# Kernel tuning notes

Hardware: AMD Instinct MI355X
Metric: run time of the kernel (lower is better)

Reference implementation:

```python
import jax, jax.numpy as jnp
import numpy as np

B, S, D, H = 4, 1024, 1024, 16
DK = D // H
EPS = 1e-6


def setup_inputs() -> dict:
    key = jax.random.key(0)
    ks = jax.random.split(key, 12)
    s = 1.0 / np.sqrt(D)
    inp = {
        "query": jax.random.normal(ks[0], (B, S, D), jnp.float32),
        "key": jax.random.normal(ks[1], (B, S, D), jnp.float32),
        "value": jax.random.normal(ks[2], (B, S, D), jnp.float32),
        "Wq": jax.random.normal(ks[3], (D, D), jnp.float32) * s,
        "bq": jnp.zeros((D,), jnp.float32),
        "Wk": jax.random.normal(ks[4], (D, D), jnp.float32) * s,
        "bk": jnp.zeros((D,), jnp.float32),
        "Wv": jax.random.normal(ks[5], (D, D), jnp.float32) * s,
        "bv": jnp.zeros((D,), jnp.float32),
        "Wo": jax.random.normal(ks[6], (D, D), jnp.float32) * s,
        "bo": jnp.zeros((D,), jnp.float32),
        "gamma": jnp.ones((D,), jnp.float32),
        "beta": jnp.zeros((D,), jnp.float32),
    }
    return inp


def reference(query, key, value, Wq, bq, Wk, bk, Wv, bv, Wo, bo, gamma, beta):
    residual = query
    # QKV projections, split into heads: [B,S,D] -> [B,H,S,DK]
    q = (query @ Wq + bq).reshape(B, S, H, DK).transpose(0, 2, 1, 3)
    k = (key @ Wk + bk).reshape(B, S, H, DK).transpose(0, 2, 1, 3)
    v = (value @ Wv + bv).reshape(B, S, H, DK).transpose(0, 2, 1, 3)
    # scaled dot-product attention (dropout is identity in eval mode)
    scores = jnp.einsum("bhqd,bhkd->bhqk", q, k) / jnp.sqrt(jnp.float32(DK))
    attn = jax.nn.softmax(scores, axis=-1)  # [B,H,S,S]
    x = jnp.einsum("bhqk,bhkd->bhqd", attn, v)
    x = x.transpose(0, 2, 1, 3).reshape(B, S, D)
    # residual + LayerNorm(eps=1e-6)
    x = x + residual
    mu = jnp.mean(x, axis=-1, keepdims=True)
    var = jnp.mean(jnp.square(x - mu), axis=-1, keepdims=True)
    x = (x - mu) * jax.lax.rsqrt(var + EPS) * gamma + beta
    out = x @ Wo + bo
    return (out, attn)
```

## Files before the change

kernel.cpp:

```cpp
#include <hip/hip_runtime.h>

typedef unsigned short u16;
typedef __attribute__((ext_vector_type(8))) short bf16x8;
typedef __attribute__((ext_vector_type(4))) float f32x4;

struct __align__(8) us4 { u16 x, y, z, w; };

#define B_  4
#define S_  1024
#define D_  1024
#define H_  16
#define DK_ 64

__device__ __forceinline__ u16 f2bf(float x) {
    union { float f; unsigned int u; } c; c.f = x;
    unsigned int r = (c.u + 0x7FFFu + ((c.u >> 16) & 1u)) >> 16;
    return (u16)r;
}

__device__ __forceinline__ u16 f2bf_trunc(float x) {
    union { float f; unsigned int u; } c; c.f = x;
    return (u16)(c.u >> 16);
}

__device__ __forceinline__ float bf2f(u16 x) {
    union { unsigned int u; float f; } c; c.u = ((unsigned int)x) << 16;
    return c.f;
}

__device__ __forceinline__ void gload_lds16(const void* g, void* l) {
    __builtin_amdgcn_global_load_lds(
        (const __attribute__((address_space(1))) unsigned int*)g,
        (__attribute__((address_space(3))) unsigned int*)l, 16, 0, 0);
}

__device__ __forceinline__ void nt_store4(f32x4 v, float* p) {
    __builtin_nontemporal_store(v, (f32x4*)p);
}

__global__ __launch_bounds__(256) void cvt_x(const float* __restrict__ q,
                                             const float* __restrict__ k,
                                             const float* __restrict__ v,
                                             u16* __restrict__ xq,
                                             u16* __restrict__ xk,
                                             u16* __restrict__ xv) {
    const float* src = (blockIdx.y == 0) ? q : (blockIdx.y == 1) ? k : v;
    u16* dst        = (blockIdx.y == 0) ? xq : (blockIdx.y == 1) ? xk : xv;
    int idx = (blockIdx.x * 256 + threadIdx.x) * 4;
    f32x4 f = *(const f32x4*)(src + idx);
    us4 o; o.x = f2bf(f[0]); o.y = f2bf(f[1]); o.z = f2bf(f[2]); o.w = f2bf(f[3]);
    *(us4*)(dst + idx) = o;
}

__global__ __launch_bounds__(256) void cvt_w(const float* __restrict__ w0, const float* __restrict__ w1,
                                             const float* __restrict__ w2, const float* __restrict__ w3,
                                             u16* __restrict__ t0, u16* __restrict__ t1,
                                             u16* __restrict__ t2, u16* __restrict__ t3) {
    __shared__ float t[64][65];
    const float* W = (blockIdx.z == 0) ? w0 : (blockIdx.z == 1) ? w1 : (blockIdx.z == 2) ? w2 : w3;
    u16* T        = (blockIdx.z == 0) ? t0 : (blockIdx.z == 1) ? t1 : (blockIdx.z == 2) ? t2 : t3;
    int k0 = blockIdx.x * 64, n0 = blockIdx.y * 64;
    int tid = threadIdx.x;
    int r4 = tid >> 6, c = tid & 63;
#pragma unroll
    for (int i = 0; i < 16; i++) {
        int r = i * 4 + r4;
        t[r][c] = W[(size_t)(k0 + r) * 1024 + n0 + c];
    }
    __syncthreads();
#pragma unroll
    for (int i = 0; i < 16; i++) {
        int r = i * 4 + r4;
        T[(size_t)(n0 + r) * 1024 + k0 + c] = f2bf(t[c][r]);
    }
}

template <int BN, int MODE>
__device__ __forceinline__ void gemm_core(const u16* __restrict__ X, const u16* __restrict__ WT,
                                          const float* __restrict__ bias, void* __restrict__ outp,
                                          float scale, int bm, int bn) {
    constexpr int NS = BN / 32;
    extern __shared__ u16 smem[];
    u16* Al = smem;
    u16* Bl = smem + 128 * 64;
    int tid = threadIdx.x, l = tid & 63, w = tid >> 6;
    int lr = l & 15, lq = l >> 4;
    int wm = (w >> 1) * 64, wn = (w & 1) * (BN / 2);
    f32x4 acc[4][NS] = {};
    for (int kk = 0; kk < 1024; kk += 64) {
        __syncthreads();
#pragma unroll
        for (int i = 0; i < 4; i++) {
            int flat = tid * 16 + i * 4096;
            int row = flat >> 7, kb = flat & 127;
            int kbs = kb ^ ((row & 7) << 4);
            gload_lds16((const char*)X + ((size_t)(bm * 128 + row) * 2048 + (size_t)kk * 2 + kbs),
                        (char*)Al + flat);
        }
#pragma unroll
        for (int i = 0; i < BN / 32; i++) {
            int flat = tid * 16 + i * 4096;
            int row = flat >> 7, kb = flat & 127;
            int kbs = kb ^ ((row & 7) << 4);
            gload_lds16((const char*)WT + ((size_t)(bn * BN + row) * 2048 + (size_t)kk * 2 + kbs),
                        (char*)Bl + flat);
        }
        asm volatile("s_waitcnt vmcnt(0)" ::: "memory");
        __syncthreads();
#pragma unroll
        for (int kkk = 0; kkk < 2; kkk++) {
            bf16x8 af[4], bfr[NS];
            int colb = kkk * 64 + lq * 16;
#pragma unroll
            for (int ms = 0; ms < 4; ms++) {
                int row = wm + ms * 16 + lr;
                af[ms] = *(const bf16x8*)((const char*)Al + row * 128 + (colb ^ ((row & 7) << 4)));
            }
#pragma unroll
            for (int ns = 0; ns < NS; ns++) {
                int row = wn + ns * 16 + lr;
                bfr[ns] = *(const bf16x8*)((const char*)Bl + row * 128 + (colb ^ ((row & 7) << 4)));
            }
#pragma unroll
            for (int ms = 0; ms < 4; ms++)
#pragma unroll
                for (int ns = 0; ns < NS; ns++) {
                    if (MODE == 1)
                        acc[ms][ns] = __builtin_amdgcn_mfma_f32_16x16x32_bf16(af[ms], bfr[ns], acc[ms][ns], 0, 0, 0);
                    else
                        acc[ms][ns] = __builtin_amdgcn_mfma_f32_16x16x32_bf16(bfr[ns], af[ms], acc[ms][ns], 0, 0, 0);
                }
        }
    }
    if (MODE == 1) {
#pragma unroll
        for (int ns = 0; ns < NS; ns++) {
            int n = bn * BN + wn + ns * 16 + lr;
            float bv_ = bias[n];
            int h = n >> 6, dk = n & 63;
#pragma unroll
            for (int ms = 0; ms < 4; ms++) {
                int mbase = bm * 128 + wm + ms * 16 + lq * 4;
                u16* o = (u16*)outp;
                int b = mbase >> 10, s0 = mbase & 1023;
                us4 pk;
                pk.x = f2bf(acc[ms][ns][0] + bv_);
                pk.y = f2bf(acc[ms][ns][1] + bv_);
                pk.z = f2bf(acc[ms][ns][2] + bv_);
                pk.w = f2bf(acc[ms][ns][3] + bv_);
                *(us4*)(o + ((size_t)(b * H_ + h) * 64 + dk) * 1024 + s0) = pk;
            }
        }
    } else {
#pragma unroll
        for (int ns = 0; ns < NS; ns++) {
            int n0 = bn * BN + wn + ns * 16 + lq * 4;
            f32x4 bv4 = *(const f32x4*)(bias + n0);
#pragma unroll
            for (int ms = 0; ms < 4; ms++) {
                int m = bm * 128 + wm + ms * 16 + lr;
                if (MODE == 0) {
                    u16* o = (u16*)outp;
                    int h = n0 >> 6, dk = n0 & 63;
                    int b = m >> 10, s = m & 1023;
                    us4 pk;
                    pk.x = f2bf((acc[ms][ns][0] + bv4[0]) * scale);
                    pk.y = f2bf((acc[ms][ns][1] + bv4[1]) * scale);
                    pk.z = f2bf((acc[ms][ns][2] + bv4[2]) * scale);
                    pk.w = f2bf((acc[ms][ns][3] + bv4[3]) * scale);
                    *(us4*)(o + ((size_t)(b * H_ + h) * 1024 + s) * 64 + dk) = pk;
                } else {
                    float* o = (float*)outp;
                    f32x4 o4 = acc[ms][ns] + bv4;
                    *(f32x4*)(o + (size_t)m * 1024 + n0) = o4;
                }
            }
        }
    }
}

__global__ __launch_bounds__(256, 3) void gemm_qkv(const u16* __restrict__ Xq, const u16* __restrict__ Xk,
                                                   const u16* __restrict__ Xv,
                                                   const u16* __restrict__ Wq, const u16* __restrict__ Wk,
                                                   const u16* __restrict__ Wv,
                                                   const float* __restrict__ bq, const float* __restrict__ bk,
                                                   const float* __restrict__ bv,
                                                   u16* __restrict__ Qh, u16* __restrict__ Kh,
                                                   u16* __restrict__ VT) {
    int z = blockIdx.z;
    const u16* X = (z == 0) ? Xq : (z == 1) ? Xk : Xv;
    const u16* W = (z == 0) ? Wq : (z == 1) ? Wk : Wv;
    const float* bia = (z == 0) ? bq : (z == 1) ? bk : bv;
    if (z == 2)
        gemm_core<128, 1>(X, W, bia, (void*)VT, 1.0f, blockIdx.x, blockIdx.y);
    else if (z == 0)
        gemm_core<128, 0>(X, W, bia, (void*)Qh, 0.125f, blockIdx.x, blockIdx.y);
    else
        gemm_core<128, 0>(X, W, bia, (void*)Kh, 1.0f, blockIdx.x, blockIdx.y);
}

__global__ __launch_bounds__(256, 3) void gemm_out(const u16* __restrict__ X, const u16* __restrict__ WT,
                                                   const float* __restrict__ bias, float* __restrict__ outp) {
    gemm_core<64, 2>(X, WT, bias, outp, 1.0f, blockIdx.x, blockIdx.y);
}

__global__ __launch_bounds__(256, 4) void attn_fused(const u16* __restrict__ Qh, const u16* __restrict__ Kh,
                                                     const u16* __restrict__ VT,
                                                     float* __restrict__ attn_out, float* __restrict__ x_out) {
    __shared__ u16 P_lds[16 * 1024];
    __shared__ float reds[4][16];
    int tid = threadIdx.x, l = tid & 63, w = tid >> 6;
    int lr = l & 15, lq = l >> 4;
    int wg = blockIdx.x;
    int xcd = wg & 7;
    int rest = wg >> 3;
    int q0 = (rest & 63) * 16;
    int bh = ((rest >> 6) << 3) | xcd;
    const u16* qp = Qh + (size_t)bh * 65536;
    const u16* kp = Kh + (size_t)bh * 65536;
    const u16* vp = VT + (size_t)bh * 65536;

    bf16x8 bq0 = *(const bf16x8*)(qp + (q0 + lr) * 64 + lq * 8);
    bf16x8 bq1 = *(const bf16x8*)(qp + (q0 + lr) * 64 + 32 + lq * 8);

    float s = 0.f;
#pragma unroll 4
    for (int n = 0; n < 16; n++) {
        int kb = w * 256 + n * 16;
        bf16x8 a0 = *(const bf16x8*)(kp + (size_t)(kb + lr) * 64 + lq * 8);
        bf16x8 a1 = *(const bf16x8*)(kp + (size_t)(kb + lr) * 64 + 32 + lq * 8);
        f32x4 a = {};
        a = __builtin_amdgcn_mfma_f32_16x16x32_bf16(a0, bq0, a, 0, 0, 0);
        a = __builtin_amdgcn_mfma_f32_16x16x32_bf16(a1, bq1, a, 0, 0, 0);
        f32x4 e;
        e[0] = __expf(a[0]); e[1] = __expf(a[1]); e[2] = __expf(a[2]); e[3] = __expf(a[3]);
        s += e[0] + e[1] + e[2] + e[3];
        int col = w * 256 + n * 16 + lq * 4;
        us4 pk;
        pk.x = f2bf_trunc(e[0]); pk.y = f2bf_trunc(e[1]);
        pk.z = f2bf_trunc(e[2]); pk.w = f2bf_trunc(e[3]);
        *(us4*)&P_lds[lr * 1024 + (col ^ ((lr & 7) << 3))] = pk;
    }
    s += __shfl_xor(s, 16);
    s += __shfl_xor(s, 32);
    if (l < 16) reds[w][lr] = s;
    __syncthreads();

    f32x4 pv0 = {}, pv1 = {};
#pragma unroll 8
    for (int kk = 0; kk < 32; kk += 2) {
        bf16x8 ap0 = *(const bf16x8*)&P_lds[lr * 1024 + ((kk * 32 + lq * 8) ^ ((lr & 7) << 3))];
        bf16x8 bv0 = *(const bf16x8*)(vp + (size_t)(w * 16 + lr) * 1024 + kk * 32 + lq * 8);
        pv0 = __builtin_amdgcn_mfma_f32_16x16x32_bf16(ap0, bv0, pv0, 0, 0, 0);
        bf16x8 ap1 = *(const bf16x8*)&P_lds[lr * 1024 + (((kk + 1) * 32 + lq * 8) ^ ((lr & 7) << 3))];
        bf16x8 bv1 = *(const bf16x8*)(vp + (size_t)(w * 16 + lr) * 1024 + (kk + 1) * 32 + lq * 8);
        pv1 = __builtin_amdgcn_mfma_f32_16x16x32_bf16(ap1, bv1, pv1, 0, 0, 0);
    }
    pv0 += pv1;

    int b = bh >> 4, h = bh & 15;
#pragma unroll
    for (int r = 0; r < 4; r++) {
        int row = lq * 4 + r;
        float inv = 1.0f / (reds[0][row] + reds[1][row] + reds[2][row] + reds[3][row]);
        __builtin_nontemporal_store(pv0[r] * inv,
            x_out + ((size_t)(b * 1024 + q0 + row)) * 1024 + h * 64 + w * 16 + lr);
    }

    size_t abase = (size_t)bh * 1048576 + (size_t)q0 * 1024;
#pragma unroll
    for (int i = 0; i < 16; i++) {
        float inv_i = 1.0f / (reds[0][i] + reds[1][i] + reds[2][i] + reds[3][i]);
        us4 pk4 = *(const us4*)&P_lds[i * 1024 + ((tid * 4) ^ ((i & 7) << 3))];
        f32x4 o;
        o[0] = bf2f(pk4.x) * inv_i;
        o[1] = bf2f(pk4.y) * inv_i;
        o[2] = bf2f(pk4.z) * inv_i;
        o[3] = bf2f(pk4.w) * inv_i;
        nt_store4(o, attn_out + abase + (size_t)i * 1024 + tid * 4);
    }
}

__global__ __launch_bounds__(256) void ln_kernel(const float* __restrict__ x, const float* __restrict__ resid,
                                                 const float* __restrict__ gamma, const float* __restrict__ beta,
                                                 u16* __restrict__ out) {
    __shared__ float as_[4], as2_[4];
    int row = blockIdx.x, tid = threadIdx.x;
    int l = tid & 63, w = tid >> 6;
    size_t base = (size_t)row * 1024 + tid * 4;
    f32x4 v = *(const f32x4*)(x + base);
    f32x4 rz = *(const f32x4*)(resid + base);
    v += rz;
    float s = v[0] + v[1] + v[2] + v[3];
    float s2 = v[0] * v[0] + v[1] * v[1] + v[2] * v[2] + v[3] * v[3];
#pragma unroll
    for (int off = 1; off < 64; off <<= 1) {
        s += __shfl_xor(s, off);
        s2 += __shfl_xor(s2, off);
    }
    if (l == 0) { as_[w] = s; as2_[w] = s2; }
    __syncthreads();
    s = as_[0] + as_[1] + as_[2] + as_[3];
    s2 = as2_[0] + as2_[1] + as2_[2] + as2_[3];
    float mean = s * (1.f / 1024.f);
    float var = s2 * (1.f / 1024.f) - mean * mean;
    float rs = rsqrtf(var + 1e-6f);
    f32x4 g = *(const f32x4*)(gamma + tid * 4);
    f32x4 bt = *(const f32x4*)(beta + tid * 4);
    us4 o;
    o.x = f2bf((v[0] - mean) * rs * g[0] + bt[0]);
    o.y = f2bf((v[1] - mean) * rs * g[1] + bt[1]);
    o.z = f2bf((v[2] - mean) * rs * g[2] + bt[2]);
    o.w = f2bf((v[3] - mean) * rs * g[3] + bt[3]);
    *(us4*)(out + base) = o;
}

extern "C" void kernel_launch(void* const* d_in, const int* in_sizes, int n_in,
                              void* d_out, int out_size, void* d_ws, size_t ws_size,
                              hipStream_t stream) {
    const float* query = (const float*)d_in[0];
    const float* key   = (const float*)d_in[1];
    const float* value = (const float*)d_in[2];
    const float* Wq    = (const float*)d_in[3];
    const float* bq    = (const float*)d_in[4];
    const float* Wk    = (const float*)d_in[5];
    const float* bk    = (const float*)d_in[6];
    const float* Wv    = (const float*)d_in[7];
    const float* bv    = (const float*)d_in[8];
    const float* Wo    = (const float*)d_in[9];
    const float* bo    = (const float*)d_in[10];
    const float* gamma = (const float*)d_in[11];
    const float* beta  = (const float*)d_in[12];

    char* ws = (char*)d_ws;
    u16* XQ  = (u16*)(ws + 0);
    u16* XK  = (u16*)(ws + 8388608);
    u16* XV  = (u16*)(ws + 16777216);
    u16* WQT = (u16*)(ws + 25165824);
    u16* WKT = (u16*)(ws + 27262976);
    u16* WVT = (u16*)(ws + 29360128);
    u16* WOT = (u16*)(ws + 31457280);
    u16* Qh  = (u16*)(ws + 33554432);
    u16* Kh  = (u16*)(ws + 41943040);
    u16* VT  = (u16*)(ws + 50331648);
    float* PV = (float*)(ws + 0);
    u16* LN  = (u16*)(ws + 16777216);

    float* outp = (float*)d_out;
    float* attn = outp + 4194304;

    cvt_x<<<dim3(4096, 3), 256, 0, stream>>>(query, key, value, XQ, XK, XV);
    cvt_w<<<dim3(16, 16, 4), 256, 0, stream>>>(Wq, Wk, Wv, Wo, WQT, WKT, WVT, WOT);
    gemm_qkv<<<dim3(32, 8, 3), 256, 32768, stream>>>(XQ, XK, XV, WQT, WKT, WVT, bq, bk, bv, Qh, Kh, VT);
    attn_fused<<<dim3(4096), 256, 0, stream>>>(Qh, Kh, VT, attn, PV);
    ln_kernel<<<4096, 256, 0, stream>>>(PV, query, gamma, beta, LN);
    gemm_out<<<dim3(32, 16), 256, 24576, stream>>>(LN, WOT, bo, outp);
}
```

Baseline: 204.8 us.

## Process 32 query rows per attention block and store attn before PV

The attention kernel now handles 32 query rows per 512-thread block instead of 16 per 256-thread block. Each K and V tile fetched by a block is reused across twice as many queries, and the block count is halved. The normalized attention probabilities are written out before the PV matmul instead of after, which could overlap the large attn stores with PV compute. The LDS footprint doubles to 64KB, which limits how many blocks fit per CU and may reduce occupancy.

Result: no change. 208.3 us (+1.7%).

```diff
diff --git a/kernel.cpp b/kernel.cpp
--- a/kernel.cpp
+++ b/kernel.cpp
@@ -204,80 +204,91 @@
     gemm_core<64, 2>(X, WT, bias, outp, 1.0f, blockIdx.x, blockIdx.y);
 }
 
-__global__ __launch_bounds__(256, 4) void attn_fused(const u16* __restrict__ Qh, const u16* __restrict__ Kh,
+__global__ __launch_bounds__(512, 4) void attn_fused(const u16* __restrict__ Qh, const u16* __restrict__ Kh,
                                                      const u16* __restrict__ VT,
                                                      float* __restrict__ attn_out, float* __restrict__ x_out) {
-    __shared__ u16 P_lds[16 * 1024];
-    __shared__ float reds[4][16];
+    __shared__ u16 P_lds[32 * 1024];
+    __shared__ float reds[4][32];
     int tid = threadIdx.x, l = tid & 63, w = tid >> 6;
     int lr = l & 15, lq = l >> 4;
     int wg = blockIdx.x;
     int xcd = wg & 7;
     int rest = wg >> 3;
-    int q0 = (rest & 63) * 16;
-    int bh = ((rest >> 6) << 3) | xcd;
+    int q0 = (rest & 31) * 32;
+    int bh = ((rest >> 5) << 3) | xcd;
     const u16* qp = Qh + (size_t)bh * 65536;
     const u16* kp = Kh + (size_t)bh * 65536;
     const u16* vp = VT + (size_t)bh * 65536;
 
-    bf16x8 bq0 = *(const bf16x8*)(qp + (q0 + lr) * 64 + lq * 8);
-    bf16x8 bq1 = *(const bf16x8*)(qp + (q0 + lr) * 64 + 32 + lq * 8);
+    int ks = w >> 1;
+    int h2 = w & 1;
+    int qrow = h2 * 16 + lr;
+
+    bf16x8 bq0 = *(const bf16x8*)(qp + (q0 + qrow) * 64 + lq * 8);
+    bf16x8 bq1 = *(const bf16x8*)(qp + (q0 + qrow) * 64 + 32 + lq * 8);
 
     float s = 0.f;
 #pragma unroll 4
     for (int n = 0; n < 16; n++) {
-        int kb = w * 256 + n * 16;
+        int kb = ks * 256 + n * 16;
         bf16x8 a0 = *(const bf16x8*)(kp + (size_t)(kb + lr) * 64 + lq * 8);
         bf16x8 a1 = *(const bf16x8*)(kp + (size_t)(kb + lr) * 64 + 32 + lq * 8);
         f32x4 a = {};
         a = __builtin_amdgcn_mfma_f32_16x16x32_bf16(a0, bq0, a, 0, 0, 0);
         a = __builtin_amdgcn_mfma_f32_16x16x32_bf16(a1, bq1, a, 0, 0, 0);
         f32x4 e;
-        e[0] = __expf(a[0]); e[1] = __expf(a[1]); e[2] = __expf(a[2]); e[3] = __expf(a[3]);
+        e[0] = __expf(a[0]); e[1] = __expf(a[1]);
+        e[2] = __expf(a[2]); e[3] = __expf(a[3]);
         s += e[0] + e[1] + e[2] + e[3];
-        int col = w * 256 + n * 16 + lq * 4;
+        int col = ks * 256 + n * 16 + lq * 4;
         us4 pk;
         pk.x = f2bf_trunc(e[0]); pk.y = f2bf_trunc(e[1]);
         pk.z = f2bf_trunc(e[2]); pk.w = f2bf_trunc(e[3]);
-        *(us4*)&P_lds[lr * 1024 + (col ^ ((lr & 7) << 3))] = pk;
+        *(us4*)&P_lds[qrow * 1024 + (col ^ ((qrow & 7) << 3))] = pk;
     }
     s += __shfl_xor(s, 16);
     s += __shfl_xor(s, 32);
-    if (l < 16) reds[w][lr] = s;
+    if (l < 16) reds[ks][qrow] = s;
     __syncthreads();
 
-    f32x4 pv0 = {}, pv1 = {};
-#pragma unroll 8
-    for (int kk = 0; kk < 32; kk += 2) {
-        bf16x8 ap0 = *(const bf16x8*)&P_lds[lr * 1024 + ((kk * 32 + lq * 8) ^ ((lr & 7) << 3))];
-        bf16x8 bv0 = *(const bf16x8*)(vp + (size_t)(w * 16 + lr) * 1024 + kk * 32 + lq * 8);
-        pv0 = __builtin_amdgcn_mfma_f32_16x16x32_bf16(ap0, bv0, pv0, 0, 0, 0);
-        bf16x8 ap1 = *(const bf16x8*)&P_lds[lr * 1024 + (((kk + 1) * 32 + lq * 8) ^ ((lr & 7) << 3))];
-        bf16x8 bv1 = *(const bf16x8*)(vp + (size_t)(w * 16 + lr) * 1024 + (kk + 1) * 32 + lq * 8);
-        pv1 = __builtin_amdgcn_mfma_f32_16x16x32_bf16(ap1, bv1, pv1, 0, 0, 0);
-    }
-    pv0 += pv1;
-
-    int b = bh >> 4, h = bh & 15;
-#pragma unroll
-    for (int r = 0; r < 4; r++) {
-        int row = lq * 4 + r;
-        float inv = 1.0f / (reds[0][row] + reds[1][row] + reds[2][row] + reds[3][row]);
-        __builtin_nontemporal_store(pv0[r] * inv,
-            x_out + ((size_t)(b * 1024 + q0 + row)) * 1024 + h * 64 + w * 16 + lr);
-    }
-
     size_t abase = (size_t)bh * 1048576 + (size_t)q0 * 1024;
-#pragma unroll
-    for (int i = 0; i < 16; i++) {
+    int half = tid >> 8;
+    int c4 = (tid & 255) * 4;
+#pragma unroll
+    for (int ii = 0; ii < 16; ii++) {
+        int i = ii * 2 + half;
         float inv_i = 1.0f / (reds[0][i] + reds[1][i] + reds[2][i] + reds[3][i]);
-        us4 pk4 = *(const us4*)&P_lds[i * 1024 + ((tid * 4) ^ ((i & 7) << 3))];
+        us4 pk4 = *(const us4*)&P_lds[i * 1024 + (c4 ^ ((i & 7) << 3))];
         f32x4 o;
         o[0] = bf2f(pk4.x) * inv_i;
         o[1] = bf2f(pk4.y) * inv_i;
         o[2] = bf2f(pk4.z) * inv_i;
         o[3] = bf2f(pk4.w) * inv_i;
-        nt_store4(o, attn_out + abase + (size_t)i * 1024 + tid * 4);
+        nt_store4(o, attn_out + abase + (size_t)i * 1024 + c4);
+    }
+
+    int rh = w & 1;
+    int ds = (w >> 1) * 16;
+    f32x4 pv0 = {}, pv1 = {};
+#pragma unroll 8
+    for (int kk = 0; kk < 32; kk += 2) {
+        int prow = rh * 16 + lr;
+        bf16x8 ap0 = *(const bf16x8*)&P_lds[prow * 1024 + ((kk * 32 + lq * 8) ^ ((prow & 7) << 3))];
+        bf16x8 bv0 = *(const bf16x8*)(vp + (size_t)(ds + lr) * 1024 + kk * 32 + lq * 8);
+        pv0 = __builtin_amdgcn_mfma_f32_16x16x32_bf16(ap0, bv0, pv0, 0, 0, 0);
+        bf16x8 ap1 = *(const bf16x8*)&P_lds[prow * 1024 + (((kk + 1) * 32 + lq * 8) ^ ((prow & 7) << 3))];
+        bf16x8 bv1 = *(const bf16x8*)(vp + (size_t)(ds + lr) * 1024 + (kk + 1) * 32 + lq * 8);
+        pv1 = __builtin_amdgcn_mfma_f32_16x16x32_bf16(ap1, bv1, pv1, 0, 0, 0);
+    }
+    pv0 += pv1;
+
+    int b = bh >> 4, h = bh & 15;
+#pragma unroll
+    for (int r = 0; r < 4; r++) {
+        int row = rh * 16 + lq * 4 + r;
+        float inv = 1.0f / (reds[0][row] + reds[1][row] + reds[2][row] + reds[3][row]);
+        __builtin_nontemporal_store(pv0[r] * inv,
+            x_out + ((size_t)(b * 1024 + q0 + row)) * 1024 + h * 64 + ds + lr);
     }
 }
 
@@ -352,7 +363,7 @@
     cvt_x<<<dim3(4096, 3), 256, 0, stream>>>(query, key, value, XQ, XK, XV);
     cvt_w<<<dim3(16, 16, 4), 256, 0, stream>>>(Wq, Wk, Wv, Wo, WQT, WKT, WVT, WOT);
     gemm_qkv<<<dim3(32, 8, 3), 256, 32768, stream>>>(XQ, XK, XV, WQT, WKT, WVT, bq, bk, bv, Qh, Kh, VT);
-    attn_fused<<<dim3(4096), 256, 0, stream>>>(Qh, Kh, VT, attn, PV);
+    attn_fused<<<dim3(2048), 512, 0, stream>>>(Qh, Kh, VT, attn, PV);
     ln_kernel<<<4096, 256, 0, stream>>>(PV, query, gamma, beta, LN);
     gemm_out<<<dim3(32, 16), 256, 24576, stream>>>(LN, WOT, bo, outp);
 }
```
